# Optimization experiments

Measured on AMD Instinct MI355X. Metric: run time of the kernel, lower is better.

The kernel has to match this reference:

```python
import jax, jax.numpy as jnp
import numpy as np

NUM_GRAPHS = 128
N_NODES = 50000
N_EDGES = 400000
EMB = 384
L = 5
BN_EPS = 1e-5


def _bn(h, gamma, beta):
    # training-mode BatchNorm1d over the node/edge dim (biased variance, like torch)
    m = h.mean(axis=0)
    v = h.var(axis=0)
    return gamma * (h - m) * jax.lax.rsqrt(v + BN_EPS) + beta


def setup_inputs() -> dict:
    key = jax.random.key(0)
    ks = jax.random.split(key, 16)
    batch = jnp.sort(jax.random.randint(ks[0], (N_NODES,), 0, NUM_GRAPHS))
    x = jax.random.randint(ks[1], (N_NODES, 9), 0, 64)
    edge_index = jax.random.randint(ks[2], (2, N_EDGES), 0, N_NODES)
    edge_attr = jax.random.randint(ks[3], (N_EDGES, 3), 0, 8)
    s = 0.05
    atom_emb = jax.random.normal(ks[4], (9, 64, EMB), jnp.float32) * s
    bond_emb = jax.random.normal(ks[5], (3, 8, EMB), jnp.float32) * s
    # per-layer GINE MLP params, stacked over layers
    W1 = jax.random.normal(ks[6], (L, EMB, 2 * EMB), jnp.float32) * (1.0 / np.sqrt(EMB))
    b1 = jnp.zeros((L, 2 * EMB), jnp.float32)
    g1 = jnp.ones((L, 2 * EMB), jnp.float32)
    be1 = jnp.zeros((L, 2 * EMB), jnp.float32)
    W2 = jax.random.normal(ks[7], (L, 2 * EMB, EMB), jnp.float32) * (1.0 / np.sqrt(2 * EMB))
    b2 = jnp.zeros((L, EMB), jnp.float32)
    # outer per-layer BatchNorm params
    gbn = jnp.ones((L, EMB), jnp.float32)
    bbn = jnp.zeros((L, EMB), jnp.float32)
    return {"batch": batch, "x": x, "edge_index": edge_index, "edge_attr": edge_attr,
            "atom_emb": atom_emb, "bond_emb": bond_emb,
            "W1": W1, "b1": b1, "g1": g1, "be1": be1,
            "W2": W2, "b2": b2, "gbn": gbn, "bbn": bbn}


def reference(batch, x, edge_index, edge_attr, atom_emb, bond_emb,
              W1, b1, g1, be1, W2, b2, gbn, bbn):
    # AtomEncoder / BondEncoder: sum of per-column embedding lookups
    h = atom_emb[jnp.arange(9), x].sum(axis=1)          # [N, EMB]
    e = bond_emb[jnp.arange(3), edge_attr].sum(axis=1)  # [E, EMB]
    src, dst = edge_index[0], edge_index[1]
    for i in range(W1.shape[0]):
        # GINEConv: sum_j relu(x_j + e_ij)  (edge_weight defaults to ones)
        msg = jax.nn.relu(h[src] + e)                                   # [E, EMB]
        agg = jax.ops.segment_sum(msg, dst, num_segments=N_NODES)      # [N, EMB]
        z = h + agg                                                     # (1+eps)*x_i + agg, eps=0
        # MLP: Linear -> BN -> ReLU -> Linear
        z = z @ W1[i] + b1[i]
        z = jax.nn.relu(_bn(z, g1[i], be1[i]))
        z = z @ W2[i] + b2[i]
        # outer BN + ReLU (drop_ratio = 0.0)
        h = jax.nn.relu(_bn(z, gbn[i], bbn[i]))
    # standard pooling: global_add_pool
    graph_emb = jax.ops.segment_sum(h, batch, num_segments=NUM_GRAPHS)  # [G, EMB]
    return graph_emb, h
```

## Files before the change

### kernel.cpp

```cpp
#include <hip/hip_runtime.h>
#include <stdint.h>

#define NN 50000
#define NE 400000
#define EMB 384
#define NH 768
#define NL 5

typedef __bf16 bf16x8_t __attribute__((ext_vector_type(8)));
typedef float  f32x4_t  __attribute__((ext_vector_type(4)));

__device__ __forceinline__ float bflo(uint32_t u){ union{uint32_t u;float f;} v; v.u = u<<16; return v.f; }
__device__ __forceinline__ float bfhi(uint32_t u){ union{uint32_t u;float f;} v; v.u = u & 0xffff0000u; return v.f; }
__device__ __forceinline__ uint16_t f2bf(float f){
  union{float f;uint32_t u;} v; v.f=f;
  uint32_t r = v.u + 0x7fffu + ((v.u>>16)&1u);
  return (uint16_t)(r>>16);
}
__device__ __forceinline__ uint32_t bfpack2(float a, float b){
  return (uint32_t)f2bf(a) | ((uint32_t)f2bf(b)<<16);
}

__global__ void hist_kernel(const int* __restrict__ dst, int* __restrict__ count){
  int i = blockIdx.x*256 + threadIdx.x;
  if (i < NE) atomicAdd(&count[dst[i]], 1);
}
__global__ void scan_block_sum(const int* __restrict__ count, int* __restrict__ bsum, int n){
  __shared__ int s[256];
  int i = blockIdx.x*256 + threadIdx.x;
  s[threadIdx.x] = (i<n) ? count[i] : 0;
  __syncthreads();
  for (int st=128; st>0; st>>=1){
    if (threadIdx.x < st) s[threadIdx.x] += s[threadIdx.x+st];
    __syncthreads();
  }
  if (threadIdx.x==0) bsum[blockIdx.x] = s[0];
}
__global__ void scan_excl_small(int* __restrict__ bsum, int nb){
  __shared__ int s[256];
  int t = threadIdx.x;
  int v = (t<nb) ? bsum[t] : 0;
  s[t] = v;
  __syncthreads();
  for (int st=1; st<256; st<<=1){
    int u = (t>=st) ? s[t-st] : 0;
    __syncthreads();
    s[t] += u;
    __syncthreads();
  }
  if (t<nb) bsum[t] = s[t] - v;
}
__global__ void scan_final(const int* __restrict__ count, const int* __restrict__ bsum,
                           int* __restrict__ rowptr, int* __restrict__ cursor, int n){
  __shared__ int s[256];
  int t = threadIdx.x;
  int i = blockIdx.x*256 + t;
  int v = (i<n) ? count[i] : 0;
  s[t] = v;
  __syncthreads();
  for (int st=1; st<256; st<<=1){
    int u = (t>=st) ? s[t-st] : 0;
    __syncthreads();
    s[t] += u;
    __syncthreads();
  }
  int off = bsum[blockIdx.x] + s[t] - v;
  if (i < n){
    rowptr[i] = off; cursor[i] = off;
    if (i == n-1) rowptr[n] = off + v;
  }
}
__global__ void scatter_kernel(const int* __restrict__ dst, const int* __restrict__ src,
                               const int* __restrict__ eattr, int* __restrict__ cursor,
                               int* __restrict__ csr_src, int* __restrict__ csr_code){
  int e = blockIdx.x*256 + threadIdx.x;
  if (e < NE){
    int p = atomicAdd(&cursor[dst[e]], 1);
    csr_src[p] = src[e];
    csr_code[p] = eattr[e*3] | (eattr[e*3+1]<<3) | (eattr[e*3+2]<<6);
  }
}

__global__ void build_bond(const float* __restrict__ bemb, uint16_t* __restrict__ bt){
  const int code = blockIdx.x;
  const int t0 = code&7, t1=(code>>3)&7, t2=code>>6;
  const int c = threadIdx.x;
  const float2 a = ((const float2*)(bemb + (size_t)( 0+t0)*EMB))[c];
  const float2 b = ((const float2*)(bemb + (size_t)( 8+t1)*EMB))[c];
  const float2 d = ((const float2*)(bemb + (size_t)(16+t2)*EMB))[c];
  ((uint32_t*)(bt + (size_t)code*EMB))[c] = bfpack2(a.x+b.x+d.x, a.y+b.y+d.y);
}

__global__ void transpose_w(const float* __restrict__ in, uint16_t* __restrict__ outp,
                            int R, int Cc){
  __shared__ float tile[32][33];
  const size_t lo = (size_t)blockIdx.z * R * Cc;
  int cb = blockIdx.x*32, rb = blockIdx.y*32;
  int r = rb + threadIdx.y, c = cb + threadIdx.x;
  if (r < R && c < Cc) tile[threadIdx.y][threadIdx.x] = in[lo + (size_t)r*Cc + c];
  __syncthreads();
  int orr = cb + threadIdx.y, occ = rb + threadIdx.x;
  if (orr < Cc && occ < R) outp[lo + (size_t)orr*R + occ] = f2bf(tile[threadIdx.x][threadIdx.y]);
}

__global__ __launch_bounds__(256) void atom_encode(
    const int* __restrict__ x, const float* __restrict__ aemb,
    uint16_t* __restrict__ h){
  const int w = threadIdx.x >> 6, lane = threadIdx.x & 63;
  const int i = blockIdx.x*4 + w;
  if (i >= NN) return;
  float a0=0,a1=0,a2=0,a3=0,a4=0,a5=0;
  #pragma unroll
  for (int k=0;k<9;k++){
    const int idx = x[i*9+k];
    const float2* p = (const float2*)(aemb + ((size_t)(k*64+idx))*EMB) + lane*3;
    float2 u0=p[0], u1=p[1], u2=p[2];
    a0+=u0.x; a1+=u0.y; a2+=u1.x; a3+=u1.y; a4+=u2.x; a5+=u2.y;
  }
  uint32_t* hp = (uint32_t*)(h + (size_t)i*EMB) + lane*3;
  hp[0]=bfpack2(a0,a1); hp[1]=bfpack2(a2,a3); hp[2]=bfpack2(a4,a5);
}

template<int BNREL>
__global__ __launch_bounds__(256) void agg_kernel(
    const uint16_t* __restrict__ in, const uint16_t* __restrict__ bondt,
    const float* __restrict__ scale, const float* __restrict__ shift,
    const int* __restrict__ rowptr, const int* __restrict__ csr_src,
    const int* __restrict__ csr_code, uint16_t* __restrict__ za){
  const int w = threadIdx.x >> 6, lane = threadIdx.x & 63;
  const int i = blockIdx.x*4 + w;
  if (i >= NN) return;

  float sc0=0,sc1=0,sc2=0,sc3=0,sc4=0,sc5=0, sh0=0,sh1=0,sh2=0,sh3=0,sh4=0,sh5=0;
  if (BNREL){
    const int c = lane*6;
    sc0=scale[c]; sc1=scale[c+1]; sc2=scale[c+2]; sc3=scale[c+3]; sc4=scale[c+4]; sc5=scale[c+5];
    sh0=shift[c]; sh1=shift[c+1]; sh2=shift[c+2]; sh3=shift[c+3]; sh4=shift[c+4]; sh5=shift[c+5];
  }

  const uint32_t* hs = (const uint32_t*)(in + (size_t)i*EMB) + lane*3;
  uint32_t s0=hs[0], s1=hs[1], s2=hs[2];
  float a0,a1,a2,a3,a4,a5;
  if (BNREL){
    a0 = fmaxf(bflo(s0)*sc0+sh0, 0.f); a1 = fmaxf(bfhi(s0)*sc1+sh1, 0.f);
    a2 = fmaxf(bflo(s1)*sc2+sh2, 0.f); a3 = fmaxf(bfhi(s1)*sc3+sh3, 0.f);
    a4 = fmaxf(bflo(s2)*sc4+sh4, 0.f); a5 = fmaxf(bfhi(s2)*sc5+sh5, 0.f);
  } else {
    a0 = bflo(s0); a1 = bfhi(s0); a2 = bflo(s1); a3 = bfhi(s1); a4 = bflo(s2); a5 = bfhi(s2);
  }

  const int rs = rowptr[i], re = rowptr[i+1];
  int k = rs;
  for (; k + 4 <= re; k += 4){
    int sj[4], cj[4];
    #pragma unroll
    for (int j=0;j<4;j++){ sj[j]=csr_src[k+j]; cj[j]=csr_code[k+j]; }
    uint32_t u[4][3], b[4][3];
    #pragma unroll
    for (int j=0;j<4;j++){
      const uint32_t* hp = (const uint32_t*)(in + (size_t)sj[j]*EMB) + lane*3;
      u[j][0]=hp[0]; u[j][1]=hp[1]; u[j][2]=hp[2];
      const uint32_t* bp = (const uint32_t*)(bondt + (size_t)cj[j]*EMB) + lane*3;
      b[j][0]=bp[0]; b[j][1]=bp[1]; b[j][2]=bp[2];
    }
    #pragma unroll
    for (int j=0;j<4;j++){
      float v0,v1,v2,v3,v4,v5;
      if (BNREL){
        v0 = fmaxf(bflo(u[j][0])*sc0+sh0, 0.f); v1 = fmaxf(bfhi(u[j][0])*sc1+sh1, 0.f);
        v2 = fmaxf(bflo(u[j][1])*sc2+sh2, 0.f); v3 = fmaxf(bfhi(u[j][1])*sc3+sh3, 0.f);
        v4 = fmaxf(bflo(u[j][2])*sc4+sh4, 0.f); v5 = fmaxf(bfhi(u[j][2])*sc5+sh5, 0.f);
      } else {
        v0=bflo(u[j][0]); v1=bfhi(u[j][0]); v2=bflo(u[j][1]);
        v3=bfhi(u[j][1]); v4=bflo(u[j][2]); v5=bfhi(u[j][2]);
      }
      a0 += fmaxf(v0+bflo(b[j][0]), 0.f); a1 += fmaxf(v1+bfhi(b[j][0]), 0.f);
      a2 += fmaxf(v2+bflo(b[j][1]), 0.f); a3 += fmaxf(v3+bfhi(b[j][1]), 0.f);
      a4 += fmaxf(v4+bflo(b[j][2]), 0.f); a5 += fmaxf(v5+bfhi(b[j][2]), 0.f);
    }
  }
  for (; k < re; k++){
    const int s = csr_src[k];
    const int code = csr_code[k];
    const uint32_t* hp = (const uint32_t*)(in + (size_t)s*EMB) + lane*3;
    uint32_t u0=hp[0], u1=hp[1], u2=hp[2];
    const uint32_t* bp = (const uint32_t*)(bondt + (size_t)code*EMB) + lane*3;
    uint32_t b0=bp[0], b1=bp[1], b2=bp[2];
    float v0,v1,v2,v3,v4,v5;
    if (BNREL){
      v0 = fmaxf(bflo(u0)*sc0+sh0, 0.f); v1 = fmaxf(bfhi(u0)*sc1+sh1, 0.f);
      v2 = fmaxf(bflo(u1)*sc2+sh2, 0.f); v3 = fmaxf(bfhi(u1)*sc3+sh3, 0.f);
      v4 = fmaxf(bflo(u2)*sc4+sh4, 0.f); v5 = fmaxf(bfhi(u2)*sc5+sh5, 0.f);
    } else {
      v0=bflo(u0); v1=bfhi(u0); v2=bflo(u1); v3=bfhi(u1); v4=bflo(u2); v5=bfhi(u2);
    }
    a0 += fmaxf(v0+bflo(b0), 0.f); a1 += fmaxf(v1+bfhi(b0), 0.f);
    a2 += fmaxf(v2+bflo(b1), 0.f); a3 += fmaxf(v3+bfhi(b1), 0.f);
    a4 += fmaxf(v4+bflo(b2), 0.f); a5 += fmaxf(v5+bfhi(b2), 0.f);
  }

  uint32_t* zp = (uint32_t*)(za + (size_t)i*EMB) + lane*3;
  zp[0] = bfpack2(a0,a1);
  zp[1] = bfpack2(a2,a3);
  zp[2] = bfpack2(a4,a5);
}

template<int BNA>
__global__ __launch_bounds__(256) void gemm_bt(
    const uint16_t* __restrict__ A, const uint16_t* __restrict__ Bt,
    const float* __restrict__ bias, const float* __restrict__ scA,
    const float* __restrict__ shA, uint16_t* __restrict__ C,
    float* __restrict__ stats, int M, int N, int K, int nbr){
  __shared__ __align__(16) uint16_t As[128*32];
  __shared__ __align__(16) uint16_t Bs[128*32];
  __shared__ float sAs[BNA ? NH : 1];
  __shared__ float hAs[BNA ? NH : 1];
  __shared__ float csum[128];
  __shared__ float csq[128];

  const int tid = threadIdx.x;
  const int nbc = N >> 7;
  const int xcd = blockIdx.x & 7;
  const int slot = blockIdx.x >> 3;
  const int bcol = slot % nbc;
  const int brow = (slot / nbc)*8 + xcd;
  if (brow >= nbr) return;
  const int rowbase = brow << 7;

  const int lane = tid & 63;
  const int w = tid >> 6;
  const int wm = w >> 1, wn = w & 1;
  const int quad = lane >> 4, l16 = lane & 15;

  const int s0 = tid, s1 = 256 + tid;
  const int kq0 = s0 >> 7, r0 = s0 & 127;
  const int kq1 = s1 >> 7, r1 = s1 & 127;
  int gra0 = rowbase + r0; if (gra0 >= M) gra0 = M-1;
  int gra1 = rowbase + r1; if (gra1 >= M) gra1 = M-1;
  const int pb0 = bcol*128 + (r0 & 64) + ((r0 & 15) << 2) + ((r0 >> 4) & 3);
  const int pb1 = bcol*128 + (r1 & 64) + ((r1 & 15) << 2) + ((r1 >> 4) & 3);

  const uint16_t* gA0 = A + (size_t)gra0*K + kq0*8;
  const uint16_t* gA1 = A + (size_t)gra1*K + kq1*8;
  const uint16_t* gB0 = Bt + (size_t)pb0*K + kq0*8;
  const uint16_t* gB1 = Bt + (size_t)pb1*K + kq1*8;

  uint4 ra0 = *(const uint4*)gA0;
  uint4 ra1 = *(const uint4*)gA1;
  uint4 rb0 = *(const uint4*)gB0;
  uint4 rb1 = *(const uint4*)gB1;

  if (BNA){
    for (int i = tid; i < K; i += 256){ sAs[i] = scA[i]; hAs[i] = shA[i]; }
    __syncthreads();
  }

  f32x4_t acc[4][4];
  #pragma unroll
  for (int mi=0;mi<4;mi++)
    #pragma unroll
    for (int ni=0;ni<4;ni++)
      acc[mi][ni] = (f32x4_t){0.f,0.f,0.f,0.f};

  for (int k0 = 0; k0 < K; k0 += 32){
    if (!BNA){
      *(uint4*)&As[s0*8] = ra0;
      *(uint4*)&As[s1*8] = ra1;
    } else {
      uint32_t in0[4] = {ra0.x,ra0.y,ra0.z,ra0.w};
      uint32_t in1[4] = {ra1.x,ra1.y,ra1.z,ra1.w};
      uint32_t o0[4], o1[4];
      const int kb0 = k0 + kq0*8, kb1 = k0 + kq1*8;
      #pragma unroll
      for (int j=0;j<4;j++){
        float x0 = fmaxf(bflo(in0[j])*sAs[kb0+2*j  ]+hAs[kb0+2*j  ], 0.f);
        float x1 = fmaxf(bfhi(in0[j])*sAs[kb0+2*j+1]+hAs[kb0+2*j+1], 0.f);
        o0[j] = bfpack2(x0,x1);
        float y0 = fmaxf(bflo(in1[j])*sAs[kb1+2*j  ]+hAs[kb1+2*j  ], 0.f);
        float y1 = fmaxf(bfhi(in1[j])*sAs[kb1+2*j+1]+hAs[kb1+2*j+1], 0.f);
        o1[j] = bfpack2(y0,y1);
      }
      *(uint4*)&As[s0*8] = make_uint4(o0[0],o0[1],o0[2],o0[3]);
      *(uint4*)&As[s1*8] = make_uint4(o1[0],o1[1],o1[2],o1[3]);
    }
    *(uint4*)&Bs[s0*8] = rb0;
    *(uint4*)&Bs[s1*8] = rb1;
    __syncthreads();

    if (k0 + 32 < K){
      const int kn = k0 + 32;
      ra0 = *(const uint4*)(gA0 + kn);
      ra1 = *(const uint4*)(gA1 + kn);
      rb0 = *(const uint4*)(gB0 + kn);
      rb1 = *(const uint4*)(gB1 + kn);
    }

    bf16x8_t fa[4], fb[4];
    #pragma unroll
    for (int mi=0;mi<4;mi++)
      fa[mi] = *(const bf16x8_t*)&As[(quad*128 + wm*64 + mi*16 + l16)*8];
    #pragma unroll
    for (int ni=0;ni<4;ni++)
      fb[ni] = *(const bf16x8_t*)&Bs[(quad*128 + wn*64 + ni*16 + l16)*8];
    #pragma unroll
    for (int mi=0;mi<4;mi++)
      #pragma unroll
      for (int ni=0;ni<4;ni++)
        acc[mi][ni] = __builtin_amdgcn_mfma_f32_16x16x32_bf16(fa[mi], fb[ni], acc[mi][ni], 0,0,0);
    __syncthreads();
  }

  if (tid < 128){ csum[tid]=0.f; csq[tid]=0.f; }
  __syncthreads();

  const int lcol = wn*64 + l16*4;
  const int colbase = bcol*128 + lcol;
  float bv[4], ssum[4] = {0,0,0,0}, sq[4] = {0,0,0,0};
  #pragma unroll
  for (int ni=0;ni<4;ni++) bv[ni] = bias[colbase + ni];

  #pragma unroll
  for (int mi=0;mi<4;mi++){
    #pragma unroll
    for (int r=0;r<4;r++){
      const int grow = rowbase + wm*64 + mi*16 + quad*4 + r;
      if (grow < M){
        float v0 = acc[mi][0][r] + bv[0];
        float v1 = acc[mi][1][r] + bv[1];
        float v2 = acc[mi][2][r] + bv[2];
        float v3 = acc[mi][3][r] + bv[3];
        uint2 pk = make_uint2(bfpack2(v0,v1), bfpack2(v2,v3));
        *(uint2*)(C + (size_t)grow*N + colbase) = pk;
        ssum[0]+=v0; ssum[1]+=v1; ssum[2]+=v2; ssum[3]+=v3;
        sq[0]+=v0*v0; sq[1]+=v1*v1; sq[2]+=v2*v2; sq[3]+=v3*v3;
      }
    }
  }
  #pragma unroll
  for (int ni=0;ni<4;ni++){
    ssum[ni] += __shfl_xor(ssum[ni], 16); ssum[ni] += __shfl_xor(ssum[ni], 32);
    sq[ni]   += __shfl_xor(sq[ni],   16); sq[ni]   += __shfl_xor(sq[ni],   32);
  }
  if (quad == 0){
    #pragma unroll
    for (int ni=0;ni<4;ni++){
      atomicAdd(&csum[lcol + ni], ssum[ni]);
      atomicAdd(&csq [lcol + ni], sq[ni]);
    }
  }
  __syncthreads();
  if (tid < 128){
    atomicAdd(&stats[bcol*128 + tid], csum[tid]);
    atomicAdd(&stats[N + bcol*128 + tid], csq[tid]);
  }
}

__global__ void bn_finalize(const float* __restrict__ stats, const float* __restrict__ gamma,
                            const float* __restrict__ beta, float* __restrict__ scale,
                            float* __restrict__ shift, int n, float invM){
  int c = blockIdx.x*256 + threadIdx.x;
  if (c < n){
    float mean = stats[c]*invM;
    float var  = stats[n+c]*invM - mean*mean;
    float sc = gamma[c] * rsqrtf(var + 1e-5f);
    scale[c] = sc;
    shift[c] = beta[c] - mean*sc;
  }
}

__global__ void bn_relu_final(const uint16_t* __restrict__ u, const float* __restrict__ scale,
                              const float* __restrict__ shift, float* __restrict__ hf){
  int i = blockIdx.x*256 + threadIdx.x;
  const int total2 = NN*EMB/2;
  if (i >= total2) return;
  uint32_t v = ((const uint32_t*)u)[i];
  int c = (i*2) % EMB;
  float f0 = fmaxf(bflo(v)*scale[c  ] + shift[c  ], 0.f);
  float f1 = fmaxf(bfhi(v)*scale[c+1] + shift[c+1], 0.f);
  ((float2*)hf)[i] = make_float2(f0, f1);
}

__global__ void pool_kernel(const float* __restrict__ h, const int* __restrict__ batch,
                            float* __restrict__ pool){
  __shared__ int bs[64];
  int c = threadIdx.x;
  int n0 = blockIdx.x*64;
  if (c < 64){ int i = n0 + c; bs[c] = (i < NN) ? batch[i] : -1; }
  __syncthreads();
  float sum = 0.f; int cur = -1;
  for (int tt=0; tt<64; tt++){
    int i = n0 + tt;
    if (i >= NN) break;
    int g = bs[tt];
    float v = h[(size_t)i*EMB + c];
    if (g != cur){
      if (cur >= 0) atomicAdd(&pool[(size_t)cur*EMB + c], sum);
      cur = g; sum = v;
    } else sum += v;
  }
  if (cur >= 0) atomicAdd(&pool[(size_t)cur*EMB + c], sum);
}
__global__ void pool_to_out(const float* __restrict__ pool, float* __restrict__ outp){
  int i = blockIdx.x*256 + threadIdx.x;
  if (i < 128*EMB) outp[i] = pool[i];
}

extern "C" void kernel_launch(void* const* d_in, const int* in_sizes, int n_in,
                              void* d_out, int out_size, void* d_ws, size_t ws_size,
                              hipStream_t stream){
  (void)in_sizes; (void)n_in; (void)out_size; (void)ws_size;
  const int* batch = (const int*)d_in[0];
  const int* x     = (const int*)d_in[1];
  const int* eidx  = (const int*)d_in[2];
  const int* eattr = (const int*)d_in[3];
  const float* aemb = (const float*)d_in[4];
  const float* bemb = (const float*)d_in[5];
  const float* W1 = (const float*)d_in[6];
  const float* b1 = (const float*)d_in[7];
  const float* g1 = (const float*)d_in[8];
  const float* be1= (const float*)d_in[9];
  const float* W2 = (const float*)d_in[10];
  const float* b2 = (const float*)d_in[11];
  const float* gbn= (const float*)d_in[12];
  const float* bbn= (const float*)d_in[13];
  float* out = (float*)d_out;

  char* base = (char*)d_ws;
  size_t off = 0;
  auto alloc = [&](size_t bytes) -> void* {
    void* p = base + off;
    off = (off + bytes + 255) & ~(size_t)255;
    return p;
  };
  uint16_t* za   = (uint16_t*)alloc((size_t)NN*EMB*2);
  uint16_t* zm   = (uint16_t*)alloc((size_t)NN*EMB*2);
  uint16_t* t    = (uint16_t*)alloc((size_t)NN*NH*2);
  uint16_t* W1t  = (uint16_t*)alloc((size_t)NL*NH*EMB*2);
  uint16_t* W2t  = (uint16_t*)alloc((size_t)NL*EMB*NH*2);
  uint16_t* bondt= (uint16_t*)alloc((size_t)512*EMB*2);
  float* stats1  = (float*)alloc(NH*2*4);
  float* stats2  = (float*)alloc(EMB*2*4);
  float* scale1  = (float*)alloc(NH*4);
  float* shift1  = (float*)alloc(NH*4);
  float* scale2  = (float*)alloc(EMB*4);
  float* shift2  = (float*)alloc(EMB*4);
  float* pool    = (float*)alloc(128*EMB*4);
  int* count   = (int*)alloc((size_t)NN*4);
  int* rowptr  = (int*)alloc((size_t)(NN+1)*4);
  int* cursor  = (int*)alloc((size_t)NN*4);
  int* bsum    = (int*)alloc(256*4);
  int* csr_src = (int*)alloc((size_t)NE*4);
  int* csr_code= (int*)alloc((size_t)NE*4);

  const int* esrc = eidx;
  const int* edst = eidx + NE;
  const int nsb = (NN + 255)/256;

  hipMemsetAsync(count, 0, (size_t)NN*4, stream);
  hist_kernel<<<(NE+255)/256, 256, 0, stream>>>(edst, count);
  scan_block_sum<<<nsb, 256, 0, stream>>>(count, bsum, NN);
  scan_excl_small<<<1, 256, 0, stream>>>(bsum, nsb);
  scan_final<<<nsb, 256, 0, stream>>>(count, bsum, rowptr, cursor, NN);
  scatter_kernel<<<(NE+255)/256, 256, 0, stream>>>(edst, esrc, eattr, cursor, csr_src, csr_code);

  build_bond<<<512, 192, 0, stream>>>(bemb, bondt);
  transpose_w<<<dim3(NH/32, EMB/32, NL), dim3(32,32), 0, stream>>>(W1, W1t, EMB, NH);
  transpose_w<<<dim3(EMB/32, NH/32, NL), dim3(32,32), 0, stream>>>(W2, W2t, NH, EMB);

  atom_encode<<<NN/4, 256, 0, stream>>>(x, aemb, zm);
  hipMemsetAsync(pool, 0, (size_t)128*EMB*4, stream);

  const int nbr = (NN + 127)/128;
  const int nbrr = ((nbr + 7)/8)*8;
  const int g1blocks = nbrr*(NH/128);
  const int g2blocks = nbrr*(EMB/128);
  for (int l = 0; l < NL; l++){
    if (l == 0)
      agg_kernel<0><<<NN/4, 256, 0, stream>>>(zm, bondt, nullptr, nullptr,
                                              rowptr, csr_src, csr_code, za);
    else
      agg_kernel<1><<<NN/4, 256, 0, stream>>>(zm, bondt, scale2, shift2,
                                              rowptr, csr_src, csr_code, za);
    hipMemsetAsync(stats1, 0, (size_t)NH*2*4, stream);
    gemm_bt<0><<<g1blocks, 256, 0, stream>>>(
        za, W1t + (size_t)l*NH*EMB, b1 + l*NH, nullptr, nullptr, t, stats1, NN, NH, EMB, nbr);
    bn_finalize<<<(NH+255)/256, 256, 0, stream>>>(stats1, g1 + l*NH, be1 + l*NH,
                                                  scale1, shift1, NH, 1.0f/NN);
    hipMemsetAsync(stats2, 0, (size_t)EMB*2*4, stream);
    gemm_bt<1><<<g2blocks, 256, 0, stream>>>(
        t, W2t + (size_t)l*EMB*NH, b2 + l*EMB, scale1, shift1, zm, stats2, NN, EMB, NH, nbr);
    bn_finalize<<<(EMB+255)/256, 256, 0, stream>>>(stats2, gbn + l*EMB, bbn + l*EMB,
                                                   scale2, shift2, EMB, 1.0f/NN);
  }
  bn_relu_final<<<(NN*EMB/2 + 255)/256, 256, 0, stream>>>(zm, scale2, shift2, out + 128*EMB);
  pool_kernel<<<(NN+63)/64, 384, 0, stream>>>(out + 128*EMB, batch, pool);
  pool_to_out<<<(128*EMB+255)/256, 256, 0, stream>>>(pool, out);
}
```

Measured before the change: 1.349 ms.

## Enlarge GEMM row tile to 256 and fold stats zeroing into bn_finalize

The GEMM block tile grows from 128x128 to 256x128, so each wave computes a 128x64 subtile with 32 MFMA accumulators and each thread loads a full A row slice. This raises B-operand reuse and reduces the block count, at the cost of higher register and LDS use (launch bounds set to 2 blocks/CU). The per-layer memsets of the BN statistics buffers are removed; bn_finalize now zeroes the stats after reading them, with one upfront memset covering both buffers, assuming they are contiguous.

```diff
diff --git a/kernel.cpp b/kernel.cpp
--- a/kernel.cpp
+++ b/kernel.cpp
@@ -206,12 +206,12 @@
 }
 
 template<int BNA>
-__global__ __launch_bounds__(256) void gemm_bt(
+__global__ __launch_bounds__(256, 2) void gemm_bt(
     const uint16_t* __restrict__ A, const uint16_t* __restrict__ Bt,
     const float* __restrict__ bias, const float* __restrict__ scA,
     const float* __restrict__ shA, uint16_t* __restrict__ C,
     float* __restrict__ stats, int M, int N, int K, int nbr){
-  __shared__ __align__(16) uint16_t As[128*32];
+  __shared__ __align__(16) uint16_t As[256*32];
   __shared__ __align__(16) uint16_t Bs[128*32];
   __shared__ float sAs[BNA ? NH : 1];
   __shared__ float hAs[BNA ? NH : 1];
@@ -225,85 +225,77 @@
   const int bcol = slot % nbc;
   const int brow = (slot / nbc)*8 + xcd;
   if (brow >= nbr) return;
-  const int rowbase = brow << 7;
+  const int rowbase = brow << 8;
 
   const int lane = tid & 63;
   const int w = tid >> 6;
   const int wm = w >> 1, wn = w & 1;
   const int quad = lane >> 4, l16 = lane & 15;
 
-  const int s0 = tid, s1 = 256 + tid;
-  const int kq0 = s0 >> 7, r0 = s0 & 127;
-  const int kq1 = s1 >> 7, r1 = s1 & 127;
-  int gra0 = rowbase + r0; if (gra0 >= M) gra0 = M-1;
-  int gra1 = rowbase + r1; if (gra1 >= M) gra1 = M-1;
-  const int pb0 = bcol*128 + (r0 & 64) + ((r0 & 15) << 2) + ((r0 >> 4) & 3);
-  const int pb1 = bcol*128 + (r1 & 64) + ((r1 & 15) << 2) + ((r1 >> 4) & 3);
-
-  const uint16_t* gA0 = A + (size_t)gra0*K + kq0*8;
-  const uint16_t* gA1 = A + (size_t)gra1*K + kq1*8;
-  const uint16_t* gB0 = Bt + (size_t)pb0*K + kq0*8;
-  const uint16_t* gB1 = Bt + (size_t)pb1*K + kq1*8;
-
-  uint4 ra0 = *(const uint4*)gA0;
-  uint4 ra1 = *(const uint4*)gA1;
-  uint4 rb0 = *(const uint4*)gB0;
-  uint4 rb1 = *(const uint4*)gB1;
+  int gra = rowbase + tid; if (gra >= M) gra = M-1;
+  const uint16_t* gA = A + (size_t)gra*K;
+  const int rB = tid & 127, kqb = tid >> 7;
+  const int pb = bcol*128 + (rB & 64) + ((rB & 15) << 2) + ((rB >> 4) & 3);
+  const uint16_t* gB = Bt + (size_t)pb*K;
+
+  uint4 rap[4], rbp[2];
+  #pragma unroll
+  for (int j=0;j<4;j++) rap[j] = *(const uint4*)(gA + j*8);
+  rbp[0] = *(const uint4*)(gB + kqb*8);
+  rbp[1] = *(const uint4*)(gB + (kqb+2)*8);
 
   if (BNA){
     for (int i = tid; i < K; i += 256){ sAs[i] = scA[i]; hAs[i] = shA[i]; }
     __syncthreads();
   }
 
-  f32x4_t acc[4][4];
-  #pragma unroll
-  for (int mi=0;mi<4;mi++)
+  f32x4_t acc[8][4];
+  #pragma unroll
+  for (int mi=0;mi<8;mi++)
     #pragma unroll
     for (int ni=0;ni<4;ni++)
       acc[mi][ni] = (f32x4_t){0.f,0.f,0.f,0.f};
 
   for (int k0 = 0; k0 < K; k0 += 32){
     if (!BNA){
-      *(uint4*)&As[s0*8] = ra0;
-      *(uint4*)&As[s1*8] = ra1;
+      #pragma unroll
+      for (int j=0;j<4;j++) *(uint4*)&As[(j*256 + tid)*8] = rap[j];
     } else {
-      uint32_t in0[4] = {ra0.x,ra0.y,ra0.z,ra0.w};
-      uint32_t in1[4] = {ra1.x,ra1.y,ra1.z,ra1.w};
-      uint32_t o0[4], o1[4];
-      const int kb0 = k0 + kq0*8, kb1 = k0 + kq1*8;
       #pragma unroll
       for (int j=0;j<4;j++){
-        float x0 = fmaxf(bflo(in0[j])*sAs[kb0+2*j  ]+hAs[kb0+2*j  ], 0.f);
-        float x1 = fmaxf(bfhi(in0[j])*sAs[kb0+2*j+1]+hAs[kb0+2*j+1], 0.f);
-        o0[j] = bfpack2(x0,x1);
-        float y0 = fmaxf(bflo(in1[j])*sAs[kb1+2*j  ]+hAs[kb1+2*j  ], 0.f);
-        float y1 = fmaxf(bfhi(in1[j])*sAs[kb1+2*j+1]+hAs[kb1+2*j+1], 0.f);
-        o1[j] = bfpack2(y0,y1);
+        const int kb = k0 + j*8;
+        uint32_t in[4] = {rap[j].x, rap[j].y, rap[j].z, rap[j].w};
+        uint32_t o[4];
+        #pragma unroll
+        for (int q=0;q<4;q++){
+          float x0 = fmaxf(bflo(in[q])*sAs[kb+2*q  ]+hAs[kb+2*q  ], 0.f);
+          float x1 = fmaxf(bfhi(in[q])*sAs[kb+2*q+1]+hAs[kb+2*q+1], 0.f);
+          o[q] = bfpack2(x0,x1);
+        }
+        *(uint4*)&As[(j*256 + tid)*8] = make_uint4(o[0],o[1],o[2],o[3]);
       }
-      *(uint4*)&As[s0*8] = make_uint4(o0[0],o0[1],o0[2],o0[3]);
-      *(uint4*)&As[s1*8] = make_uint4(o1[0],o1[1],o1[2],o1[3]);
-    }
-    *(uint4*)&Bs[s0*8] = rb0;
-    *(uint4*)&Bs[s1*8] = rb1;
+    }
+    *(uint4*)&Bs[tid*8]       = rbp[0];
+    *(uint4*)&Bs[(256+tid)*8] = rbp[1];
     __syncthreads();
 
     if (k0 + 32 < K){
       const int kn = k0 + 32;
-      ra0 = *(const uint4*)(gA0 + kn);
-      ra1 = *(const uint4*)(gA1 + kn);
-      rb0 = *(const uint4*)(gB0 + kn);
-      rb1 = *(const uint4*)(gB1 + kn);
-    }
-
-    bf16x8_t fa[4], fb[4];
-    #pragma unroll
-    for (int mi=0;mi<4;mi++)
-      fa[mi] = *(const bf16x8_t*)&As[(quad*128 + wm*64 + mi*16 + l16)*8];
+      #pragma unroll
+      for (int j=0;j<4;j++) rap[j] = *(const uint4*)(gA + kn + j*8);
+      rbp[0] = *(const uint4*)(gB + kn + kqb*8);
+      rbp[1] = *(const uint4*)(gB + kn + (kqb+2)*8);
+    }
+
+    bf16x8_t fa[8], fb[4];
+    #pragma unroll
+    for (int mi=0;mi<8;mi++)
+      fa[mi] = *(const bf16x8_t*)&As[(quad*256 + wm*128 + mi*16 + l16)*8];
     #pragma unroll
     for (int ni=0;ni<4;ni++)
       fb[ni] = *(const bf16x8_t*)&Bs[(quad*128 + wn*64 + ni*16 + l16)*8];
     #pragma unroll
-    for (int mi=0;mi<4;mi++)
+    for (int mi=0;mi<8;mi++)
       #pragma unroll
       for (int ni=0;ni<4;ni++)
         acc[mi][ni] = __builtin_amdgcn_mfma_f32_16x16x32_bf16(fa[mi], fb[ni], acc[mi][ni], 0,0,0);
@@ -320,10 +312,10 @@
   for (int ni=0;ni<4;ni++) bv[ni] = bias[colbase + ni];
 
   #pragma unroll
-  for (int mi=0;mi<4;mi++){
+  for (int mi=0;mi<8;mi++){
     #pragma unroll
     for (int r=0;r<4;r++){
-      const int grow = rowbase + wm*64 + mi*16 + quad*4 + r;
+      const int grow = rowbase + wm*128 + mi*16 + quad*4 + r;
       if (grow < M){
         float v0 = acc[mi][0][r] + bv[0];
         float v1 = acc[mi][1][r] + bv[1];
@@ -355,7 +347,7 @@
   }
 }
 
-__global__ void bn_finalize(const float* __restrict__ stats, const float* __restrict__ gamma,
+__global__ void bn_finalize(float* __restrict__ stats, const float* __restrict__ gamma,
                             const float* __restrict__ beta, float* __restrict__ scale,
                             float* __restrict__ shift, int n, float invM){
   int c = blockIdx.x*256 + threadIdx.x;
@@ -365,6 +357,8 @@
     float sc = gamma[c] * rsqrtf(var + 1e-5f);
     scale[c] = sc;
     shift[c] = beta[c] - mean*sc;
+    stats[c] = 0.f;
+    stats[n+c] = 0.f;
   }
 }
 
@@ -469,8 +463,9 @@
 
   atom_encode<<<NN/4, 256, 0, stream>>>(x, aemb, zm);
   hipMemsetAsync(pool, 0, (size_t)128*EMB*4, stream);
-
-  const int nbr = (NN + 127)/128;
+  hipMemsetAsync(stats1, 0, (size_t)(NH*2 + EMB*2)*4, stream);
+
+  const int nbr = (NN + 255)/256;
   const int nbrr = ((nbr + 7)/8)*8;
   const int g1blocks = nbrr*(NH/128);
   const int g2blocks = nbrr*(EMB/128);
@@ -481,12 +476,10 @@
     else
       agg_kernel<1><<<NN/4, 256, 0, stream>>>(zm, bondt, scale2, shift2,
                                               rowptr, csr_src, csr_code, za);
-    hipMemsetAsync(stats1, 0, (size_t)NH*2*4, stream);
     gemm_bt<0><<<g1blocks, 256, 0, stream>>>(
         za, W1t + (size_t)l*NH*EMB, b1 + l*NH, nullptr, nullptr, t, stats1, NN, NH, EMB, nbr);
     bn_finalize<<<(NH+255)/256, 256, 0, stream>>>(stats1, g1 + l*NH, be1 + l*NH,
                                                   scale1, shift1, NH, 1.0f/NN);
-    hipMemsetAsync(stats2, 0, (size_t)EMB*2*4, stream);
     gemm_bt<1><<<g2blocks, 256, 0, stream>>>(
         t, W2t + (size_t)l*EMB*NH, b2 + l*EMB, scale1, shift1, zm, stats2, NN, EMB, NH, nbr);
     bn_finalize<<<(EMB+255)/256, 256, 0, stream>>>(stats2, gbn + l*EMB, bbn + l*EMB,
```

Result: slower. 2.025 ms (+50.1%).

## Use persistent agg kernel with atomic work counter and fold stats zeroing into finalize

Applied to the files above, without the earlier changes.

The aggregation kernel becomes persistent: a fixed grid of 2048 blocks where each wavefront repeatedly grabs the next node index from a global atomic counter, replacing one-wave-per-node static launch. This targets load imbalance from uneven node degrees and block launch overhead. Separately, the per-layer memsets of the BN stats buffers are removed; bn_finalize now zeroes the stats after reading them, and one memset up front clears stats and the per-layer counters. This relies on the workspace layout being contiguous for the single memset and adds atomic contention on the counter.

```diff
diff --git a/kernel.cpp b/kernel.cpp
--- a/kernel.cpp
+++ b/kernel.cpp
@@ -126,10 +126,9 @@
     const uint16_t* __restrict__ in, const uint16_t* __restrict__ bondt,
     const float* __restrict__ scale, const float* __restrict__ shift,
     const int* __restrict__ rowptr, const int* __restrict__ csr_src,
-    const int* __restrict__ csr_code, uint16_t* __restrict__ za){
-  const int w = threadIdx.x >> 6, lane = threadIdx.x & 63;
-  const int i = blockIdx.x*4 + w;
-  if (i >= NN) return;
+    const int* __restrict__ csr_code, uint16_t* __restrict__ za,
+    int* __restrict__ counter){
+  const int lane = threadIdx.x & 63;
 
   float sc0=0,sc1=0,sc2=0,sc3=0,sc4=0,sc5=0, sh0=0,sh1=0,sh2=0,sh3=0,sh4=0,sh5=0;
   if (BNREL){
@@ -138,71 +137,78 @@
     sh0=shift[c]; sh1=shift[c+1]; sh2=shift[c+2]; sh3=shift[c+3]; sh4=shift[c+4]; sh5=shift[c+5];
   }
 
-  const uint32_t* hs = (const uint32_t*)(in + (size_t)i*EMB) + lane*3;
-  uint32_t s0=hs[0], s1=hs[1], s2=hs[2];
-  float a0,a1,a2,a3,a4,a5;
-  if (BNREL){
-    a0 = fmaxf(bflo(s0)*sc0+sh0, 0.f); a1 = fmaxf(bfhi(s0)*sc1+sh1, 0.f);
-    a2 = fmaxf(bflo(s1)*sc2+sh2, 0.f); a3 = fmaxf(bfhi(s1)*sc3+sh3, 0.f);
-    a4 = fmaxf(bflo(s2)*sc4+sh4, 0.f); a5 = fmaxf(bfhi(s2)*sc5+sh5, 0.f);
-  } else {
-    a0 = bflo(s0); a1 = bfhi(s0); a2 = bflo(s1); a3 = bfhi(s1); a4 = bflo(s2); a5 = bfhi(s2);
-  }
-
-  const int rs = rowptr[i], re = rowptr[i+1];
-  int k = rs;
-  for (; k + 4 <= re; k += 4){
-    int sj[4], cj[4];
-    #pragma unroll
-    for (int j=0;j<4;j++){ sj[j]=csr_src[k+j]; cj[j]=csr_code[k+j]; }
-    uint32_t u[4][3], b[4][3];
-    #pragma unroll
-    for (int j=0;j<4;j++){
-      const uint32_t* hp = (const uint32_t*)(in + (size_t)sj[j]*EMB) + lane*3;
-      u[j][0]=hp[0]; u[j][1]=hp[1]; u[j][2]=hp[2];
-      const uint32_t* bp = (const uint32_t*)(bondt + (size_t)cj[j]*EMB) + lane*3;
-      b[j][0]=bp[0]; b[j][1]=bp[1]; b[j][2]=bp[2];
-    }
-    #pragma unroll
-    for (int j=0;j<4;j++){
+  for (;;){
+    int i = 0;
+    if (lane == 0) i = atomicAdd(counter, 1);
+    i = __shfl(i, 0, 64);
+    if (i >= NN) break;
+
+    const uint32_t* hs = (const uint32_t*)(in + (size_t)i*EMB) + lane*3;
+    uint32_t s0=hs[0], s1=hs[1], s2=hs[2];
+    float a0,a1,a2,a3,a4,a5;
+    if (BNREL){
+      a0 = fmaxf(bflo(s0)*sc0+sh0, 0.f); a1 = fmaxf(bfhi(s0)*sc1+sh1, 0.f);
+      a2 = fmaxf(bflo(s1)*sc2+sh2, 0.f); a3 = fmaxf(bfhi(s1)*sc3+sh3, 0.f);
+      a4 = fmaxf(bflo(s2)*sc4+sh4, 0.f); a5 = fmaxf(bfhi(s2)*sc5+sh5, 0.f);
+    } else {
+      a0 = bflo(s0); a1 = bfhi(s0); a2 = bflo(s1); a3 = bfhi(s1); a4 = bflo(s2); a5 = bfhi(s2);
+    }
+
+    const int rs = rowptr[i], re = rowptr[i+1];
+    int k = rs;
+    for (; k + 4 <= re; k += 4){
+      int sj[4], cj[4];
+      #pragma unroll
+      for (int j=0;j<4;j++){ sj[j]=csr_src[k+j]; cj[j]=csr_code[k+j]; }
+      uint32_t u[4][3], b[4][3];
+      #pragma unroll
+      for (int j=0;j<4;j++){
+        const uint32_t* hp = (const uint32_t*)(in + (size_t)sj[j]*EMB) + lane*3;
+        u[j][0]=hp[0]; u[j][1]=hp[1]; u[j][2]=hp[2];
+        const uint32_t* bp = (const uint32_t*)(bondt + (size_t)cj[j]*EMB) + lane*3;
+        b[j][0]=bp[0]; b[j][1]=bp[1]; b[j][2]=bp[2];
+      }
+      #pragma unroll
+      for (int j=0;j<4;j++){
+        float v0,v1,v2,v3,v4,v5;
+        if (BNREL){
+          v0 = fmaxf(bflo(u[j][0])*sc0+sh0, 0.f); v1 = fmaxf(bfhi(u[j][0])*sc1+sh1, 0.f);
+          v2 = fmaxf(bflo(u[j][1])*sc2+sh2, 0.f); v3 = fmaxf(bfhi(u[j][1])*sc3+sh3, 0.f);
+          v4 = fmaxf(bflo(u[j][2])*sc4+sh4, 0.f); v5 = fmaxf(bfhi(u[j][2])*sc5+sh5, 0.f);
+        } else {
+          v0=bflo(u[j][0]); v1=bfhi(u[j][0]); v2=bflo(u[j][1]);
+          v3=bfhi(u[j][1]); v4=bflo(u[j][2]); v5=bfhi(u[j][2]);
+        }
+        a0 += fmaxf(v0+bflo(b[j][0]), 0.f); a1 += fmaxf(v1+bfhi(b[j][0]), 0.f);
+        a2 += fmaxf(v2+bflo(b[j][1]), 0.f); a3 += fmaxf(v3+bfhi(b[j][1]), 0.f);
+        a4 += fmaxf(v4+bflo(b[j][2]), 0.f); a5 += fmaxf(v5+bfhi(b[j][2]), 0.f);
+      }
+    }
+    for (; k < re; k++){
+      const int s = csr_src[k];
+      const int code = csr_code[k];
+      const uint32_t* hp = (const uint32_t*)(in + (size_t)s*EMB) + lane*3;
+      uint32_t u0=hp[0], u1=hp[1], u2=hp[2];
+      const uint32_t* bp = (const uint32_t*)(bondt + (size_t)code*EMB) + lane*3;
+      uint32_t b0=bp[0], b1=bp[1], b2=bp[2];
       float v0,v1,v2,v3,v4,v5;
       if (BNREL){
-        v0 = fmaxf(bflo(u[j][0])*sc0+sh0, 0.f); v1 = fmaxf(bfhi(u[j][0])*sc1+sh1, 0.f);
-        v2 = fmaxf(bflo(u[j][1])*sc2+sh2, 0.f); v3 = fmaxf(bfhi(u[j][1])*sc3+sh3, 0.f);
-        v4 = fmaxf(bflo(u[j][2])*sc4+sh4, 0.f); v5 = fmaxf(bfhi(u[j][2])*sc5+sh5, 0.f);
+        v0 = fmaxf(bflo(u0)*sc0+sh0, 0.f); v1 = fmaxf(bfhi(u0)*sc1+sh1, 0.f);
+        v2 = fmaxf(bflo(u1)*sc2+sh2, 0.f); v3 = fmaxf(bfhi(u1)*sc3+sh3, 0.f);
+        v4 = fmaxf(bflo(u2)*sc4+sh4, 0.f); v5 = fmaxf(bfhi(u2)*sc5+sh5, 0.f);
       } else {
-        v0=bflo(u[j][0]); v1=bfhi(u[j][0]); v2=bflo(u[j][1]);
-        v3=bfhi(u[j][1]); v4=bflo(u[j][2]); v5=bfhi(u[j][2]);
+        v0=bflo(u0); v1=bfhi(u0); v2=bflo(u1); v3=bfhi(u1); v4=bflo(u2); v5=bfhi(u2);
       }
-      a0 += fmaxf(v0+bflo(b[j][0]), 0.f); a1 += fmaxf(v1+bfhi(b[j][0]), 0.f);
-      a2 += fmaxf(v2+bflo(b[j][1]), 0.f); a3 += fmaxf(v3+bfhi(b[j][1]), 0.f);
-      a4 += fmaxf(v4+bflo(b[j][2]), 0.f); a5 += fmaxf(v5+bfhi(b[j][2]), 0.f);
-    }
-  }
-  for (; k < re; k++){
-    const int s = csr_src[k];
-    const int code = csr_code[k];
-    const uint32_t* hp = (const uint32_t*)(in + (size_t)s*EMB) + lane*3;
-    uint32_t u0=hp[0], u1=hp[1], u2=hp[2];
-    const uint32_t* bp = (const uint32_t*)(bondt + (size_t)code*EMB) + lane*3;
-    uint32_t b0=bp[0], b1=bp[1], b2=bp[2];
-    float v0,v1,v2,v3,v4,v5;
-    if (BNREL){
-      v0 = fmaxf(bflo(u0)*sc0+sh0, 0.f); v1 = fmaxf(bfhi(u0)*sc1+sh1, 0.f);
-      v2 = fmaxf(bflo(u1)*sc2+sh2, 0.f); v3 = fmaxf(bfhi(u1)*sc3+sh3, 0.f);
-      v4 = fmaxf(bflo(u2)*sc4+sh4, 0.f); v5 = fmaxf(bfhi(u2)*sc5+sh5, 0.f);
-    } else {
-      v0=bflo(u0); v1=bfhi(u0); v2=bflo(u1); v3=bfhi(u1); v4=bflo(u2); v5=bfhi(u2);
-    }
-    a0 += fmaxf(v0+bflo(b0), 0.f); a1 += fmaxf(v1+bfhi(b0), 0.f);
-    a2 += fmaxf(v2+bflo(b1), 0.f); a3 += fmaxf(v3+bfhi(b1), 0.f);
-    a4 += fmaxf(v4+bflo(b2), 0.f); a5 += fmaxf(v5+bfhi(b2), 0.f);
-  }
-
-  uint32_t* zp = (uint32_t*)(za + (size_t)i*EMB) + lane*3;
-  zp[0] = bfpack2(a0,a1);
-  zp[1] = bfpack2(a2,a3);
-  zp[2] = bfpack2(a4,a5);
+      a0 += fmaxf(v0+bflo(b0), 0.f); a1 += fmaxf(v1+bfhi(b0), 0.f);
+      a2 += fmaxf(v2+bflo(b1), 0.f); a3 += fmaxf(v3+bfhi(b1), 0.f);
+      a4 += fmaxf(v4+bflo(b2), 0.f); a5 += fmaxf(v5+bfhi(b2), 0.f);
+    }
+
+    uint32_t* zp = (uint32_t*)(za + (size_t)i*EMB) + lane*3;
+    zp[0] = bfpack2(a0,a1);
+    zp[1] = bfpack2(a2,a3);
+    zp[2] = bfpack2(a4,a5);
+  }
 }
 
 template<int BNA>
@@ -355,7 +361,7 @@
   }
 }
 
-__global__ void bn_finalize(const float* __restrict__ stats, const float* __restrict__ gamma,
+__global__ void bn_finalize(float* __restrict__ stats, const float* __restrict__ gamma,
                             const float* __restrict__ beta, float* __restrict__ scale,
                             float* __restrict__ shift, int n, float invM){
   int c = blockIdx.x*256 + threadIdx.x;
@@ -365,6 +371,8 @@
     float sc = gamma[c] * rsqrtf(var + 1e-5f);
     scale[c] = sc;
     shift[c] = beta[c] - mean*sc;
+    stats[c] = 0.f;
+    stats[n+c] = 0.f;
   }
 }
 
@@ -440,6 +448,7 @@
   uint16_t* bondt= (uint16_t*)alloc((size_t)512*EMB*2);
   float* stats1  = (float*)alloc(NH*2*4);
   float* stats2  = (float*)alloc(EMB*2*4);
+  int*   counters= (int*)alloc(256);
   float* scale1  = (float*)alloc(NH*4);
   float* shift1  = (float*)alloc(NH*4);
   float* scale2  = (float*)alloc(EMB*4);
@@ -469,24 +478,24 @@
 
   atom_encode<<<NN/4, 256, 0, stream>>>(x, aemb, zm);
   hipMemsetAsync(pool, 0, (size_t)128*EMB*4, stream);
+  hipMemsetAsync(stats1, 0, (size_t)(6144 + 3072 + 256), stream);
 
   const int nbr = (NN + 127)/128;
   const int nbrr = ((nbr + 7)/8)*8;
   const int g1blocks = nbrr*(NH/128);
   const int g2blocks = nbrr*(EMB/128);
+  const int aggblocks = 2048;
   for (int l = 0; l < NL; l++){
     if (l == 0)
-      agg_kernel<0><<<NN/4, 256, 0, stream>>>(zm, bondt, nullptr, nullptr,
-                                              rowptr, csr_src, csr_code, za);
+      agg_kernel<0><<<aggblocks, 256, 0, stream>>>(zm, bondt, nullptr, nullptr,
+                                                   rowptr, csr_src, csr_code, za, counters + l);
     else
-      agg_kernel<1><<<NN/4, 256, 0, stream>>>(zm, bondt, scale2, shift2,
-                                              rowptr, csr_src, csr_code, za);
-    hipMemsetAsync(stats1, 0, (size_t)NH*2*4, stream);
+      agg_kernel<1><<<aggblocks, 256, 0, stream>>>(zm, bondt, scale2, shift2,
+                                                   rowptr, csr_src, csr_code, za, counters + l);
     gemm_bt<0><<<g1blocks, 256, 0, stream>>>(
         za, W1t + (size_t)l*NH*EMB, b1 + l*NH, nullptr, nullptr, t, stats1, NN, NH, EMB, nbr);
     bn_finalize<<<(NH+255)/256, 256, 0, stream>>>(stats1, g1 + l*NH, be1 + l*NH,
                                                   scale1, shift1, NH, 1.0f/NN);
-    hipMemsetAsync(stats2, 0, (size_t)EMB*2*4, stream);
     gemm_bt<1><<<g2blocks, 256, 0, stream>>>(
         t, W2t + (size_t)l*EMB*NH, b2 + l*EMB, scale1, shift1, zm, stats2, NN, EMB, NH, nbr);
     bn_finalize<<<(EMB+255)/256, 256, 0, stream>>>(stats2, gbn + l*EMB, bbn + l*EMB,
```

New measurement: 4.460 ms. 3.31x slower.
